# Kernel optimization log

Hardware: AMD Instinct MI355X
Metric: run time of the kernel (lower is better)

Reference implementation:

```python
import jax, jax.numpy as jnp
import numpy as np

N_NODES = 50000
N_EDGES = 1600000
D_IN = 128
D_OUT = 32
ALPHA = 0.2  # LeakyReLU negative slope


def setup_inputs() -> dict:
    key = jax.random.key(0)
    k1, k2, k3, k4, k5, k6 = jax.random.split(key, 6)
    gain = float(np.sqrt(2.0))  # relu gain, xavier_normal-style scale
    X = jax.random.normal(k1, (N_NODES, D_IN), dtype=jnp.float32)
    weights = jax.random.normal(k2, (D_IN, D_OUT), dtype=jnp.float32) * (gain * np.sqrt(2.0 / (D_IN + D_OUT)))
    a0 = jax.random.normal(k3, (1, D_OUT), dtype=jnp.float32) * (gain * np.sqrt(2.0 / (1 + D_OUT)))
    a1 = jax.random.normal(k4, (1, D_OUT), dtype=jnp.float32) * (gain * np.sqrt(2.0 / (1 + D_OUT)))
    row_idx = jax.random.randint(k5, (N_EDGES,), 0, N_NODES, dtype=jnp.int32)
    col_idx = jax.random.randint(k6, (N_EDGES,), 0, N_NODES, dtype=jnp.int32)
    return {"X": X, "weights": weights, "a0": a0, "a1": a1,
            "row_idx": row_idx, "col_idx": col_idx}


def _minmax_norm(v):
    vmin = jnp.min(v)
    vmax = jnp.max(v)
    return (v - vmin) / (vmax - vmin)


def reference(X, weights, a0, a1, row_idx, col_idx):
    # X_prime = X @ W  -> [N, D]
    X_prime = X @ weights
    # Per-node partial scores; edge score e(i->j) = a0.X_prime[i] + a1.X_prime[j]
    s0 = jnp.sum(X_prime * a0, axis=-1)  # [N]
    s1 = jnp.sum(X_prime * a1, axis=-1)  # [N]
    att = s0[row_idx] + s1[col_idx]      # [E]
    # leakyrelu -> min-max normalize over all edges -> exp
    att = jax.nn.leaky_relu(att, negative_slope=ALPHA)
    att = jnp.exp(_minmax_norm(att))
    # rows_sum = SpMM(att, ones) = per-destination-row sum of edge weights
    rows_sum = jax.ops.segment_sum(att, row_idx, num_segments=N_NODES)  # [N]
    # h_prime = SpMM(att, X_prime) / rows_sum  (dropout p=0 -> identity)
    h = jax.ops.segment_sum(att[:, None] * X_prime[col_idx], row_idx,
                            num_segments=N_NODES)  # [N, D]
    return h / rows_sum[:, None]
```

## Files before the change

kernel.cpp:

```cpp
#include <hip/hip_runtime.h>
#include <hip/hip_bf16.h>
#include <math.h>

#define N_NODES 50000
#define N_EDGES 1600000
#define D_IN 128
#define D_OUT 32
#define ALPHA 0.2f

#define NB   512
#define RPB  98
#define HRPB 49
#define CAP  4096
#define CAPH 2048
#define PT   16
#define PBK  256
#define EB   (PT * PBK)
#define XNPB 32
#define XSTR 33
#define NXB  ((N_NODES + XNPB - 1) / XNPB)
#define NPB  ((N_EDGES + EB - 1) / EB)
#define SNPB 32

__device__ __forceinline__ int enc_f(float x) {
    int i = __float_as_int(x);
    return i >= 0 ? i : (i ^ 0x7fffffff);
}
__device__ __forceinline__ float dec_f(int k) {
    return __int_as_float(k >= 0 ? k : (k ^ 0x7fffffff));
}
__device__ __forceinline__ unsigned short f2bf(float x) {
    __hip_bfloat16 h = __float2bfloat16(x);
    return *(unsigned short*)&h;
}
__device__ __forceinline__ float bf2f(unsigned short u) {
    return __uint_as_float((unsigned)u << 16);
}

__global__ __launch_bounds__(256) void k_s(const float* __restrict__ X,
                                           const float* __restrict__ W,
                                           const float* __restrict__ a0,
                                           const float* __restrict__ a1,
                                           float* __restrict__ s0,
                                           float* __restrict__ s1,
                                           int* __restrict__ minmax,
                                           int* __restrict__ gcount) {
    __shared__ float wa0[D_IN], wa1[D_IN];
    const int tid = threadIdx.x;
    if (blockIdx.x == 0) {
        if (tid == 0) {
            minmax[0] = 0x7fffffff;
            minmax[1] = (int)0x80000000;
        }
        for (int i = tid; i < NB; i += 256) gcount[i] = 0;
    }
    {
        const int k = tid & 127;
        const float4* Wr = (const float4*)(W + k * D_OUT);
        const float4* A = (const float4*)((tid < 128) ? a0 : a1);
        float acc = 0.f;
#pragma unroll
        for (int j = 0; j < 8; ++j) {
            const float4 w = Wr[j];
            const float4 a = A[j];
            acc += w.x * a.x + w.y * a.y + w.z * a.z + w.w * a.w;
        }
        if (tid < 128) wa0[k] = acc; else wa1[k] = acc;
    }
    __syncthreads();
    const int node = blockIdx.x * SNPB + (tid >> 3);
    const int l = tid & 7;
    if (node < N_NODES) {
        const float4* xr = (const float4*)(X + (size_t)node * D_IN) + l * 4;
        const float4* p4 = (const float4*)wa0 + l * 4;
        const float4* q4 = (const float4*)wa1 + l * 4;
        float v0 = 0.f, v1 = 0.f;
#pragma unroll
        for (int j = 0; j < 4; ++j) {
            const float4 x = xr[j];
            const float4 p = p4[j];
            const float4 q = q4[j];
            v0 += x.x * p.x + x.y * p.y + x.z * p.z + x.w * p.w;
            v1 += x.x * q.x + x.y * q.y + x.z * q.z + x.w * q.w;
        }
#pragma unroll
        for (int m = 4; m >= 1; m >>= 1) {
            v0 += __shfl_xor(v0, m);
            v1 += __shfl_xor(v1, m);
        }
        if (l == 0) { s0[node] = v0; s1[node] = v1; }
    }
}

__global__ __launch_bounds__(256, 2) void k_fused(const float* __restrict__ X,
                                                  const float* __restrict__ W,
                                                  const int* __restrict__ row,
                                                  const int* __restrict__ col,
                                                  const float* __restrict__ s0,
                                                  const float* __restrict__ s1,
                                                  unsigned short* __restrict__ Xpb,
                                                  int* __restrict__ minmax,
                                                  int* __restrict__ gcount,
                                                  uint2* __restrict__ gEdges) {
    __shared__ char smem[16384 + XNPB * XSTR * 16] __attribute__((aligned(16)));
    const int tid = threadIdx.x;
    if (blockIdx.x < NXB) {
        float4* Wl4 = (float4*)smem;
        float4* Xl4 = (float4*)(smem + 16384);
        const int node0 = blockIdx.x * XNPB;
        {
            const float4* W4 = (const float4*)W;
#pragma unroll
            for (int i = 0; i < 4; ++i) Wl4[tid + 256 * i] = W4[tid + 256 * i];
            const float4* X4 = (const float4*)X + (size_t)node0 * (D_IN / 4);
            const int lim = (min(XNPB, N_NODES - node0)) * (D_IN / 4);
#pragma unroll
            for (int i = 0; i < 4; ++i) {
                const int idx = tid + 256 * i;
                Xl4[(idx >> 5) * XSTR + (idx & 31)] =
                    (idx < lim) ? X4[idx] : make_float4(0.f, 0.f, 0.f, 0.f);
            }
        }
        __syncthreads();
        const int g = tid >> 3;
        const int l = tid & 7;
        const int node = node0 + g;
        const float4* xr = &Xl4[g * XSTR];
        float ax = 0.f, ay = 0.f, az = 0.f, aw = 0.f;
#pragma unroll 4
        for (int kk = 0; kk < D_IN / 4; ++kk) {
            const float4 xv = xr[kk];
            const float4 w0 = Wl4[(4 * kk + 0) * 8 + l];
            const float4 w1 = Wl4[(4 * kk + 1) * 8 + l];
            const float4 w2 = Wl4[(4 * kk + 2) * 8 + l];
            const float4 w3 = Wl4[(4 * kk + 3) * 8 + l];
            ax += xv.x * w0.x + xv.y * w1.x + xv.z * w2.x + xv.w * w3.x;
            ay += xv.x * w0.y + xv.y * w1.y + xv.z * w2.y + xv.w * w3.y;
            az += xv.x * w0.z + xv.y * w1.z + xv.z * w2.z + xv.w * w3.z;
            aw += xv.x * w0.w + xv.y * w1.w + xv.z * w2.w + xv.w * w3.w;
        }
        if (node < N_NODES) {
            uint2 pk;
            pk.x = ((unsigned)f2bf(ay) << 16) | f2bf(ax);
            pk.y = ((unsigned)f2bf(aw) << 16) | f2bf(az);
            ((uint2*)Xpb)[(size_t)node * 8 + l] = pk;
        }
    } else {
        int* hist = (int*)smem;
        int* lcur = (int*)(smem + 2048);
        int* smn  = (int*)(smem + 4096);
        int* smx  = (int*)(smem + 4160);
        const int bb = blockIdx.x - NXB;
        for (int i = tid; i < NB; i += PBK) hist[i] = 0;
        __syncthreads();
        const int base = bb * EB;
        unsigned px[PT];
        float    fa[PT];
        int cnt = 0;
        int kmin = 0x7fffffff, kmax = 0x80000000;
        if (base + EB <= N_EDGES) {
            int rr[PT], cc[PT];
#pragma unroll
            for (int i = 0; i < PT / 4; ++i) {
                const int4 r4 = ((const int4*)(row + base))[tid + i * PBK];
                const int4 c4 = ((const int4*)(col + base))[tid + i * PBK];
                rr[4 * i] = r4.x; rr[4 * i + 1] = r4.y;
                rr[4 * i + 2] = r4.z; rr[4 * i + 3] = r4.w;
                cc[4 * i] = c4.x; cc[4 * i + 1] = c4.y;
                cc[4 * i + 2] = c4.z; cc[4 * i + 3] = c4.w;
            }
            float sv0[PT], sv1[PT];
#pragma unroll
            for (int i = 0; i < PT; ++i) sv0[i] = s0[rr[i]];
#pragma unroll
            for (int i = 0; i < PT; ++i) sv1[i] = s1[cc[i]];
#pragma unroll
            for (int i = 0; i < PT; ++i) {
                float a = sv0[i] + sv1[i];
                a = a > 0.f ? a : ALPHA * a;
                const int k = enc_f(a);
                kmin = min(kmin, k);
                kmax = max(kmax, k);
                const unsigned b = (unsigned)rr[i] / RPB;
                const unsigned lr = (unsigned)rr[i] - b * RPB;
                px[i] = (b << 23) | (lr << 16) | (unsigned)cc[i];
                fa[i] = a;
                atomicAdd(&hist[b], 1);
            }
            cnt = PT;
        } else {
#pragma unroll
            for (int i = 0; i < PT; ++i) {
                const int e = base + i * PBK + tid;
                if (e >= N_EDGES) break;
                const int r = row[e];
                const int c = col[e];
                float a = s0[r] + s1[c];
                a = a > 0.f ? a : ALPHA * a;
                const int k = enc_f(a);
                kmin = min(kmin, k);
                kmax = max(kmax, k);
                const unsigned b = (unsigned)r / RPB;
                const unsigned lr = (unsigned)r - b * RPB;
                px[cnt] = (b << 23) | (lr << 16) | (unsigned)c;
                fa[cnt] = a;
                ++cnt;
                atomicAdd(&hist[b], 1);
            }
        }
        __syncthreads();
        for (int i = tid; i < NB; i += PBK) {
            const int h = hist[i];
            lcur[i] = h > 0 ? atomicAdd(&gcount[i], h) : 0;
        }
        __syncthreads();
        for (int j = 0; j < cnt; ++j) {
            const unsigned p = px[j];
            const unsigned b = p >> 23;
            const int pos = atomicAdd(&lcur[b], 1);
            if (pos < CAP)
                gEdges[(size_t)b * CAP + pos] =
                    make_uint2(p & 0x7FFFFFu, (unsigned)__float_as_int(fa[j]));
        }
#pragma unroll
        for (int m = 32; m >= 1; m >>= 1) {
            kmin = min(kmin, __shfl_xor(kmin, m));
            kmax = max(kmax, __shfl_xor(kmax, m));
        }
        const int wave = tid >> 6;
        if ((tid & 63) == 0) { smn[wave] = kmin; smx[wave] = kmax; }
        __syncthreads();
        if (tid == 0) {
#pragma unroll
            for (int w = 1; w < 4; ++w) {
                kmin = min(kmin, smn[w]);
                kmax = max(kmax, smx[w]);
            }
            atomicMin(&minmax[0], kmin);
            atomicMax(&minmax[1], kmax);
        }
    }
}

__global__ __launch_bounds__(512, 8) void k_bucket(const int* __restrict__ gcount,
                                                   const uint2* __restrict__ gEdges,
                                                   const unsigned short* __restrict__ Xpb,
                                                   const int* __restrict__ minmax,
                                                   float* __restrict__ out) {
    __shared__ unsigned short scol[CAPH];
    __shared__ float swt[CAPH];
    __shared__ int off[HRPB + 1];
    __shared__ int cur[HRPB];
    const int bid = blockIdx.x;
    const int b = bid >> 1;
    const int lo = (bid & 1) * HRPB;
    const int t = threadIdx.x;
    const float mn = dec_f(minmax[0]);
    const float mx = dec_f(minmax[1]);
    const float inv = 1.0f / (mx - mn);
    const int cnt = min(gcount[b], CAP);
    const uint2* eb = gEdges + (size_t)b * CAP;

    if (t < HRPB) cur[t] = 0;
    __syncthreads();
    for (int i = t; i < cnt; i += 512) {
        const int lrl = (int)(eb[i].x >> 16) - lo;
        if ((unsigned)lrl < (unsigned)HRPB) atomicAdd(&cur[lrl], 1);
    }
    __syncthreads();
    if (t == 0) {
        int run = 0;
#pragma unroll
        for (int r = 0; r < HRPB; ++r) { off[r] = run; run += cur[r]; }
        off[HRPB] = run;
    }
    __syncthreads();
    if (t < HRPB) cur[t] = off[t];
    __syncthreads();
    for (int i = t; i < cnt; i += 512) {
        const uint2 e = eb[i];
        const int lrl = (int)(e.x >> 16) - lo;
        if ((unsigned)lrl < (unsigned)HRPB) {
            const int p = atomicAdd(&cur[lrl], 1);
            if (p < CAPH) {
                scol[p] = (unsigned short)(e.x & 0xFFFFu);
                swt[p] = __expf((__int_as_float(e.y) - mn) * inv);
            }
        }
    }
    __syncthreads();

    const int proc = t >> 5;
    const int d = t & 31;
    for (int lrl = proc; lrl < HRPB; lrl += 16) {
        const int s = min(off[lrl], CAPH);
        const int e2 = min(off[lrl + 1], CAPH);
        float ac0 = 0.f, ac1 = 0.f, ac2 = 0.f, ac3 = 0.f;
        float w0s = 0.f, w1s = 0.f, w2s = 0.f, w3s = 0.f;
        int i = s;
        for (; i + 3 < e2; i += 4) {
            const int c0 = scol[i];
            const int c1 = scol[i + 1];
            const int c2 = scol[i + 2];
            const int c3 = scol[i + 3];
            const float w0 = swt[i];
            const float w1 = swt[i + 1];
            const float w2 = swt[i + 2];
            const float w3 = swt[i + 3];
            ac0 += w0 * bf2f(Xpb[(size_t)c0 * D_OUT + d]);
            ac1 += w1 * bf2f(Xpb[(size_t)c1 * D_OUT + d]);
            ac2 += w2 * bf2f(Xpb[(size_t)c2 * D_OUT + d]);
            ac3 += w3 * bf2f(Xpb[(size_t)c3 * D_OUT + d]);
            w0s += w0; w1s += w1; w2s += w2; w3s += w3;
        }
        for (; i < e2; ++i) {
            const float w0 = swt[i];
            ac0 += w0 * bf2f(Xpb[(size_t)scol[i] * D_OUT + d]);
            w0s += w0;
        }
        const int r = b * RPB + lo + lrl;
        if (r < N_NODES)
            out[(size_t)r * D_OUT + d] =
                (ac0 + ac1 + ac2 + ac3) / (w0s + w1s + w2s + w3s);
    }
}

extern "C" void kernel_launch(void* const* d_in, const int* in_sizes, int n_in,
                              void* d_out, int out_size, void* d_ws, size_t ws_size,
                              hipStream_t stream) {
    const float* X  = (const float*)d_in[0];
    const float* W  = (const float*)d_in[1];
    const float* a0 = (const float*)d_in[2];
    const float* a1 = (const float*)d_in[3];
    const int* row  = (const int*)d_in[4];
    const int* col  = (const int*)d_in[5];
    float* out = (float*)d_out;

    float* ws = (float*)d_ws;
    int*   minmax = (int*)ws;
    int*   gcount = (int*)(ws + 64);
    float* s0 = ws + 64 + 2048;
    float* s1 = s0 + 50048;
    unsigned short* Xpb = (unsigned short*)(s1 + 50048);
    uint2* gEdges = (uint2*)(s1 + 50048 + 800000);

    k_s<<<(N_NODES + SNPB - 1) / SNPB, 256, 0, stream>>>(X, W, a0, a1, s0, s1,
                                                         minmax, gcount);
    k_fused<<<NXB + NPB, 256, 0, stream>>>(X, W, row, col, s0, s1, Xpb,
                                           minmax, gcount, gEdges);
    k_bucket<<<NB * 2, 512, 0, stream>>>(gcount, gEdges, Xpb, minmax, out);
}
```

Measured before the change: 156.2 us.

## Register-block X@W over four nodes per thread and halve edges per thread

The X@W projection now runs on only the first wavefront of each block, with each thread computing four nodes so every W value loaded from shared memory is reused four times. Separately, edges handled per thread in the partition blocks drop from 16 to 8, which doubles the number of edge blocks. The aim is to cut LDS traffic in the projection and raise parallelism or lower register pressure in the edge phase. The cost is that three of the four wavefronts sit idle during the projection, and the extra edge blocks add more atomic and histogram work.

```diff
diff --git a/kernel.cpp b/kernel.cpp
--- a/kernel.cpp
+++ b/kernel.cpp
@@ -13,7 +13,7 @@
 #define HRPB 49
 #define CAP  4096
 #define CAPH 2048
-#define PT   16
+#define PT   8
 #define PBK  256
 #define EB   (PT * PBK)
 #define XNPB 32
@@ -35,6 +35,14 @@
 }
 __device__ __forceinline__ float bf2f(unsigned short u) {
     return __uint_as_float((unsigned)u << 16);
+}
+__device__ __forceinline__ void fma4(float4& acc, const float4 x,
+                                     const float4 w0, const float4 w1,
+                                     const float4 w2, const float4 w3) {
+    acc.x += x.x * w0.x + x.y * w1.x + x.z * w2.x + x.w * w3.x;
+    acc.y += x.x * w0.y + x.y * w1.y + x.z * w2.y + x.w * w3.y;
+    acc.z += x.x * w0.z + x.y * w1.z + x.z * w2.z + x.w * w3.z;
+    acc.w += x.x * w0.w + x.y * w1.w + x.z * w2.w + x.w * w3.w;
 }
 
 __global__ __launch_bounds__(256) void k_s(const float* __restrict__ X,
@@ -122,28 +130,33 @@
             }
         }
         __syncthreads();
-        const int g = tid >> 3;
-        const int l = tid & 7;
-        const int node = node0 + g;
-        const float4* xr = &Xl4[g * XSTR];
-        float ax = 0.f, ay = 0.f, az = 0.f, aw = 0.f;
+        if (tid < 64) {
+            const int g = tid >> 3;
+            const int l = tid & 7;
+            float4 acc[4];
+#pragma unroll
+            for (int j = 0; j < 4; ++j) acc[j] = make_float4(0.f, 0.f, 0.f, 0.f);
 #pragma unroll 4
-        for (int kk = 0; kk < D_IN / 4; ++kk) {
-            const float4 xv = xr[kk];
-            const float4 w0 = Wl4[(4 * kk + 0) * 8 + l];
-            const float4 w1 = Wl4[(4 * kk + 1) * 8 + l];
-            const float4 w2 = Wl4[(4 * kk + 2) * 8 + l];
-            const float4 w3 = Wl4[(4 * kk + 3) * 8 + l];
-            ax += xv.x * w0.x + xv.y * w1.x + xv.z * w2.x + xv.w * w3.x;
-            ay += xv.x * w0.y + xv.y * w1.y + xv.z * w2.y + xv.w * w3.y;
-            az += xv.x * w0.z + xv.y * w1.z + xv.z * w2.z + xv.w * w3.z;
-            aw += xv.x * w0.w + xv.y * w1.w + xv.z * w2.w + xv.w * w3.w;
-        }
-        if (node < N_NODES) {
-            uint2 pk;
-            pk.x = ((unsigned)f2bf(ay) << 16) | f2bf(ax);
-            pk.y = ((unsigned)f2bf(aw) << 16) | f2bf(az);
-            ((uint2*)Xpb)[(size_t)node * 8 + l] = pk;
+            for (int kk = 0; kk < D_IN / 4; ++kk) {
+                const float4 w0 = Wl4[(4 * kk + 0) * 8 + l];
+                const float4 w1 = Wl4[(4 * kk + 1) * 8 + l];
+                const float4 w2 = Wl4[(4 * kk + 2) * 8 + l];
+                const float4 w3 = Wl4[(4 * kk + 3) * 8 + l];
+                fma4(acc[0], Xl4[(g +  0) * XSTR + kk], w0, w1, w2, w3);
+                fma4(acc[1], Xl4[(g +  8) * XSTR + kk], w0, w1, w2, w3);
+                fma4(acc[2], Xl4[(g + 16) * XSTR + kk], w0, w1, w2, w3);
+                fma4(acc[3], Xl4[(g + 24) * XSTR + kk], w0, w1, w2, w3);
+            }
+#pragma unroll
+            for (int j = 0; j < 4; ++j) {
+                const int node = node0 + g + 8 * j;
+                if (node < N_NODES) {
+                    uint2 pk;
+                    pk.x = ((unsigned)f2bf(acc[j].y) << 16) | f2bf(acc[j].x);
+                    pk.y = ((unsigned)f2bf(acc[j].w) << 16) | f2bf(acc[j].z);
+                    ((uint2*)Xpb)[(size_t)node * 8 + l] = pk;
+                }
+            }
         }
     } else {
         int* hist = (int*)smem;
```

Result: slower. 164.2 us (+5.2%).
